# Kernel tuning notes

Hardware: AMD Instinct MI355X
Metric: run time of the kernel (lower is better)

## Reference

```python
import jax, jax.numpy as jnp
import numpy as np

B, T, E, H = 4, 4096, 1024, 64

def setup_inputs() -> dict:
    key = jax.random.key(0)
    kx, kk, kq, kv = jax.random.split(key, 4)
    x = jax.random.normal(kx, (B, T, E), dtype=jnp.float32)
    Wk = jax.random.normal(kk, (E, H), dtype=jnp.float32) * (E ** -0.5)
    Wq = jax.random.normal(kq, (E, H), dtype=jnp.float32) * (E ** -0.5)
    Wv = jax.random.normal(kv, (E, H), dtype=jnp.float32) * (E ** -0.5)
    return {"x": x, "Wk": Wk, "Wq": Wq, "Wv": Wv}

def reference(x, Wk, Wq, Wv):
    # x: [B, T, E]; single causal attention head, dropout rate 0 (no-op)
    t = x.shape[1]
    k = jnp.einsum('bte,eh->bth', x, Wk)  # [B,T,H]
    q = jnp.einsum('bte,eh->bth', x, Wq)  # [B,T,H]
    v = jnp.einsum('bte,eh->bth', x, Wv)  # [B,T,H]
    scores = jnp.einsum('bqh,bkh->bqk', q, k) * (k.shape[-1] ** -0.5)  # [B,T,T]
    causal = jnp.tril(jnp.ones((t, t), dtype=bool))
    scores = jnp.where(causal, scores, -jnp.inf)
    attn = jax.nn.softmax(scores, axis=-1)
    return jnp.einsum('bqk,bkh->bqh', attn, v)  # [B,T,H]
```

## Files before the change

kernel.cpp:

```cpp
#include <hip/hip_runtime.h>
#include <hip/hip_bf16.h>

typedef short short8 __attribute__((ext_vector_type(8)));
typedef short short4v __attribute__((ext_vector_type(4)));
typedef float float4v __attribute__((ext_vector_type(4)));
typedef float f32x4 __attribute__((ext_vector_type(4)));

#define NEG_HUGE (-1e30f)
#define QK_SCALE 0.1803368801111204f

__device__ __forceinline__ unsigned short f2bf(float f) {
  union { __hip_bfloat16 h; unsigned short u; } c;
  c.h = __float2bfloat16(f);
  return c.u;
}

#define MFMA16(a, b, c) __builtin_amdgcn_mfma_f32_16x16x32_bf16((a), (b), (c), 0, 0, 0)

__global__ __launch_bounds__(256) void wtrans_kernel(
    const float* __restrict__ Wk, const float* __restrict__ Wq,
    const float* __restrict__ Wv, unsigned short* __restrict__ Wt) {
  int mat = blockIdx.x >> 4, kb = blockIdx.x & 15;
  const float* W = (mat == 0) ? Wk : ((mat == 1) ? Wq : Wv);
  float qscale = (mat == 1) ? QK_SCALE : 1.0f;
  __shared__ float tile[64][65];
  int tid = threadIdx.x;
  int n = tid & 63, k0 = tid >> 6;
#pragma unroll
  for (int i = 0; i < 16; i++) {
    int k = i * 4 + k0;
    tile[k][n] = W[(kb * 64 + k) * 64 + n];
  }
  __syncthreads();
  int n2 = tid >> 2, c = tid & 3;
  unsigned short tmp[16];
#pragma unroll
  for (int j = 0; j < 16; j++) tmp[j] = f2bf(tile[c * 16 + j][n2] * qscale);
  unsigned short* dst = Wt + (mat * 64 + n2) * 1024 + kb * 64 + c * 16;
  *(short8*)dst = *(short8*)tmp;
  *(short8*)(dst + 8) = *(short8*)(tmp + 8);
}

__global__ __launch_bounds__(256, 4) void proj_kernel(
    const float* __restrict__ x, const unsigned short* __restrict__ Wt,
    unsigned short* __restrict__ Kb, unsigned short* __restrict__ Qb,
    unsigned short* __restrict__ Vt) {
  __shared__ unsigned short x_lds[32][40];
  __shared__ unsigned short w_lds[192][40];
  int tid = threadIdx.x;
  int w = tid >> 6, lane = tid & 63;
  int wm = w & 1, wn = w >> 1;
  int g = lane >> 4, r = lane & 15;
  int row0 = blockIdx.x * 32;

  int xr = tid >> 3, c4 = tid & 7;
  const float* xp = &x[(size_t)(row0 + xr) * 1024 + c4 * 4];

  f32x4 acc[6];
#pragma unroll
  for (int nf = 0; nf < 6; nf++) acc[nf] = (f32x4){0.f, 0.f, 0.f, 0.f};

  float4v xv = *(const float4v*)xp;
  short8 wv[3];
#pragma unroll
  for (int i = 0; i < 3; i++) {
    int idx = tid + i * 256;
    int wr = idx >> 2, c = idx & 3;
    wv[i] = *(const short8*)&Wt[wr * 1024 + c * 8];
  }

  for (int k0 = 0; k0 < 1024; k0 += 32) {
    {
      unsigned short t4[4];
      t4[0] = f2bf(xv[0]); t4[1] = f2bf(xv[1]); t4[2] = f2bf(xv[2]); t4[3] = f2bf(xv[3]);
      *(short4v*)&x_lds[xr][c4 * 4] = *(short4v*)t4;
    }
#pragma unroll
    for (int i = 0; i < 3; i++) {
      int idx = tid + i * 256;
      int wr = idx >> 2, c = idx & 3;
      *(short8*)&w_lds[wr][c * 8] = wv[i];
    }
    if (k0 + 32 < 1024) {
      xv = *(const float4v*)(xp + k0 + 32);
#pragma unroll
      for (int i = 0; i < 3; i++) {
        int idx = tid + i * 256;
        int wr = idx >> 2, c = idx & 3;
        wv[i] = *(const short8*)&Wt[wr * 1024 + k0 + 32 + c * 8];
      }
    }
    __syncthreads();
    short8 a = *(short8*)&x_lds[wm * 16 + r][g * 8];
#pragma unroll
    for (int nf = 0; nf < 6; nf++) {
      short8 bf = *(short8*)&w_lds[wn * 96 + nf * 16 + r][g * 8];
      acc[nf] = MFMA16(a, bf, acc[nf]);
    }
    __syncthreads();
  }
#pragma unroll
  for (int nf = 0; nf < 6; nf++) {
    int col = wn * 96 + nf * 16 + r;
    if (col < 128) {
      int mat = col >> 6, h = col & 63;
      unsigned short* dst = (mat == 0) ? Kb : Qb;
#pragma unroll
      for (int reg = 0; reg < 4; reg++) {
        int grow = row0 + wm * 16 + g * 4 + reg;
        dst[(size_t)grow * 64 + h] = f2bf(acc[nf][reg]);
      }
    } else {
      int h = col & 63;
      int grow0 = row0 + wm * 16 + g * 4;
      unsigned short t4[4];
#pragma unroll
      for (int reg = 0; reg < 4; reg++) t4[reg] = f2bf(acc[nf][reg]);
      int kv6 = grow0 & 63;
      int nfb = (kv6 >> 4) & 3, gb = (kv6 >> 2) & 3;
      int s0 = (nfb >> 1) * 32 + gb * 8 + (nfb & 1) * 4;
      size_t off = ((size_t)(grow0 >> 12) * 64 + h) * 4096 +
                   ((size_t)(grow0 & 4095) & ~(size_t)63) + s0;
      *(short4v*)&Vt[off] = *(short4v*)t4;
    }
  }
}

__global__ __launch_bounds__(256, 3) void attn_kernel(
    const unsigned short* __restrict__ Kb, const unsigned short* __restrict__ Qb,
    const unsigned short* __restrict__ VtB, float* __restrict__ out) {
  __shared__ float O_l[4][32][68];
  __shared__ float st_l[4][32][2];
  int tid = threadIdx.x;
  int w = tid >> 6, lane = tid & 63;
  int g = lane >> 4, r = lane & 15;
  int bi = blockIdx.x;
  int b = bi & 3, iq = bi >> 2;
  int qt = (iq < 64) ? (64 + iq) : (127 - iq);
  int qabs = qt * 32;
  const unsigned short* Kp = Kb + (size_t)b * 4096 * 64;
  const unsigned short* Qp = Qb + (size_t)b * 4096 * 64;
  const unsigned short* Vp = VtB + (size_t)b * 64 * 4096;

  short8 qa[2][2];
#pragma unroll
  for (int mf = 0; mf < 2; mf++)
#pragma unroll
    for (int ks = 0; ks < 2; ks++)
      qa[mf][ks] = *(const short8*)&Qp[(size_t)(qabs + mf * 16 + r) * 64 + ks * 32 + g * 8];

  float m_st[2] = {NEG_HUGE, NEG_HUGE};
  float l_ln[2] = {0.f, 0.f};
  f32x4 o[4][2];
#pragma unroll
  for (int nfh = 0; nfh < 4; nfh++)
#pragma unroll
    for (int mf = 0; mf < 2; mf++) o[nfh][mf] = (f32x4){0.f, 0.f, 0.f, 0.f};

  int ntiles = (qabs >> 6) + 1;
  for (int t = w; t < ntiles; t += 4) {
    int kvb = t << 6;
    f32x4 s[4][2];
#pragma unroll
    for (int nf = 0; nf < 4; nf++)
#pragma unroll
      for (int mf = 0; mf < 2; mf++) s[nf][mf] = (f32x4){0.f, 0.f, 0.f, 0.f};
#pragma unroll
    for (int ks = 0; ks < 2; ks++) {
      short8 kf[4];
#pragma unroll
      for (int nf = 0; nf < 4; nf++)
        kf[nf] = *(const short8*)&Kp[(size_t)(kvb + nf * 16 + r) * 64 + ks * 32 + g * 8];
#pragma unroll
      for (int nf = 0; nf < 4; nf++) {
        s[nf][0] = MFMA16(kf[nf], qa[0][ks], s[nf][0]);
        s[nf][1] = MFMA16(kf[nf], qa[1][ks], s[nf][1]);
      }
    }
    short8 vf[2][4];
#pragma unroll
    for (int ks = 0; ks < 2; ks++)
#pragma unroll
      for (int nfh = 0; nfh < 4; nfh++)
        vf[ks][nfh] = *(const short8*)&Vp[(size_t)(nfh * 16 + r) * 4096 + kvb + ks * 32 + g * 8];
    if (kvb + 63 > qabs) {
#pragma unroll
      for (int mf = 0; mf < 2; mf++) {
        int q = qabs + mf * 16 + r;
#pragma unroll
        for (int nf = 0; nf < 4; nf++)
#pragma unroll
          for (int reg = 0; reg < 4; reg++) {
            int kv = kvb + nf * 16 + g * 4 + reg;
            if (kv > q) s[nf][mf][reg] = NEG_HUGE;
          }
      }
    }
    float alpha[2];
#pragma unroll
    for (int mf = 0; mf < 2; mf++) {
      float m0 = fmaxf(fmaxf(fmaxf(s[0][mf][0], s[0][mf][1]), fmaxf(s[0][mf][2], s[0][mf][3])),
                       fmaxf(fmaxf(s[1][mf][0], s[1][mf][1]), fmaxf(s[1][mf][2], s[1][mf][3])));
      float m1 = fmaxf(fmaxf(fmaxf(s[2][mf][0], s[2][mf][1]), fmaxf(s[2][mf][2], s[2][mf][3])),
                       fmaxf(fmaxf(s[3][mf][0], s[3][mf][1]), fmaxf(s[3][mf][2], s[3][mf][3])));
      float m0a = fmaxf(m0, m1);
      m0a = fmaxf(m0a, __shfl_xor(m0a, 16));
      m0a = fmaxf(m0a, __shfl_xor(m0a, 32));
      float mn = fmaxf(m_st[mf], m0a);
      alpha[mf] = exp2f(m_st[mf] - mn);
      m_st[mf] = mn;
    }
#pragma unroll
    for (int mf = 0; mf < 2; mf++) {
      float rs = 0.f;
#pragma unroll
      for (int nf = 0; nf < 4; nf++)
#pragma unroll
        for (int reg = 0; reg < 4; reg++) {
          float p = exp2f(s[nf][mf][reg] - m_st[mf]);
          s[nf][mf][reg] = p;
          rs += p;
        }
      l_ln[mf] = l_ln[mf] * alpha[mf] + rs;
#pragma unroll
      for (int nfh = 0; nfh < 4; nfh++)
#pragma unroll
        for (int reg = 0; reg < 4; reg++) o[nfh][mf][reg] *= alpha[mf];
    }
#pragma unroll
    for (int ks = 0; ks < 2; ks++)
#pragma unroll
      for (int mf = 0; mf < 2; mf++) {
        union { unsigned u[4]; short8 v; } pb;
        asm("v_cvt_pk_bf16_f32 %0, %1, %2" : "=v"(pb.u[0]) : "v"(s[2 * ks][mf][0]), "v"(s[2 * ks][mf][1]));
        asm("v_cvt_pk_bf16_f32 %0, %1, %2" : "=v"(pb.u[1]) : "v"(s[2 * ks][mf][2]), "v"(s[2 * ks][mf][3]));
        asm("v_cvt_pk_bf16_f32 %0, %1, %2" : "=v"(pb.u[2]) : "v"(s[2 * ks + 1][mf][0]), "v"(s[2 * ks + 1][mf][1]));
        asm("v_cvt_pk_bf16_f32 %0, %1, %2" : "=v"(pb.u[3]) : "v"(s[2 * ks + 1][mf][2]), "v"(s[2 * ks + 1][mf][3]));
#pragma unroll
        for (int nfh = 0; nfh < 4; nfh++)
          o[nfh][mf] = MFMA16(vf[ks][nfh], pb.v, o[nfh][mf]);
      }
  }
#pragma unroll
  for (int mf = 0; mf < 2; mf++) {
    float s0 = l_ln[mf];
    s0 += __shfl_xor(s0, 16);
    s0 += __shfl_xor(s0, 32);
    l_ln[mf] = s0;
  }
  __syncthreads();
#pragma unroll
  for (int nfh = 0; nfh < 4; nfh++)
#pragma unroll
    for (int mf = 0; mf < 2; mf++)
      *(f32x4*)&O_l[w][mf * 16 + r][nfh * 16 + g * 4] = o[nfh][mf];
  if (g == 0) {
#pragma unroll
    for (int mf = 0; mf < 2; mf++) {
      st_l[w][mf * 16 + r][0] = m_st[mf];
      st_l[w][mf * 16 + r][1] = l_ln[mf];
    }
  }
  __syncthreads();
  {
    int row = tid >> 3, cg = tid & 7;
    float mw[4], lw[4];
#pragma unroll
    for (int ww = 0; ww < 4; ww++) {
      mw[ww] = st_l[ww][row][0];
      lw[ww] = st_l[ww][row][1];
    }
    float mstar = fmaxf(fmaxf(mw[0], mw[1]), fmaxf(mw[2], mw[3]));
    float sc[4], lstar = 0.f;
#pragma unroll
    for (int ww = 0; ww < 4; ww++) { sc[ww] = exp2f(mw[ww] - mstar); lstar += sc[ww] * lw[ww]; }
    float inv = 1.0f / lstar;
    float a0[8];
#pragma unroll
    for (int cc = 0; cc < 8; cc++) a0[cc] = 0.f;
#pragma unroll
    for (int ww = 0; ww < 4; ww++) {
      f32x4 v0 = *(f32x4*)&O_l[ww][row][cg * 8];
      f32x4 v1 = *(f32x4*)&O_l[ww][row][cg * 8 + 4];
#pragma unroll
      for (int e = 0; e < 4; e++) { a0[e] += sc[ww] * v0[e]; a0[4 + e] += sc[ww] * v1[e]; }
    }
    float4v o0, o1;
#pragma unroll
    for (int e = 0; e < 4; e++) { o0[e] = a0[e] * inv; o1[e] = a0[4 + e] * inv; }
    float* op = &out[((size_t)b * 4096 + qabs + row) * 64 + cg * 8];
    *(float4v*)op = o0;
    *(float4v*)(op + 4) = o1;
  }
}

extern "C" void kernel_launch(void* const* d_in, const int* in_sizes, int n_in,
                              void* d_out, int out_size, void* d_ws, size_t ws_size,
                              hipStream_t stream) {
  (void)in_sizes; (void)n_in; (void)out_size; (void)ws_size;
  const float* x  = (const float*)d_in[0];
  const float* Wk = (const float*)d_in[1];
  const float* Wq = (const float*)d_in[2];
  const float* Wv = (const float*)d_in[3];
  float* out = (float*)d_out;
  char* ws = (char*)d_ws;

  unsigned short* Wt = (unsigned short*)ws;
  unsigned short* Kb = (unsigned short*)(ws + (512u << 10));
  unsigned short* Qb = (unsigned short*)(ws + (512u << 10) + (2u << 20));
  unsigned short* Vt = (unsigned short*)(ws + (512u << 10) + (4u << 20));

  wtrans_kernel<<<48, 256, 0, stream>>>(Wk, Wq, Wv, Wt);
  proj_kernel<<<512, 256, 0, stream>>>(x, Wt, Kb, Qb, Vt);
  attn_kernel<<<512, 256, 0, stream>>>(Kb, Qb, Vt, out);
}
```

Baseline: 62.96 us.

## Double-buffer LDS in projection kernel and widen K step to 64

Moves the QKV projection GEMM to double-buffered LDS tiles with a 64-wide K step. This halves the iteration count and needs one barrier per iteration instead of two. The next tile's global loads are issued before the MFMAs on the current tile and written to the alternate buffer afterwards, overlapping memory latency with compute. It raises LDS use and register pressure, so launch bounds drop to 2 blocks per CU.

```diff
diff --git a/kernel.cpp b/kernel.cpp
--- a/kernel.cpp
+++ b/kernel.cpp
@@ -41,61 +41,79 @@
   *(short8*)(dst + 8) = *(short8*)(tmp + 8);
 }
 
-__global__ __launch_bounds__(256, 4) void proj_kernel(
+__global__ __launch_bounds__(256, 2) void proj_kernel(
     const float* __restrict__ x, const unsigned short* __restrict__ Wt,
     unsigned short* __restrict__ Kb, unsigned short* __restrict__ Qb,
     unsigned short* __restrict__ Vt) {
-  __shared__ unsigned short x_lds[32][40];
-  __shared__ unsigned short w_lds[192][40];
+  __shared__ unsigned short x_lds[2][32][68];
+  __shared__ unsigned short w_lds[2][192][68];
   int tid = threadIdx.x;
   int w = tid >> 6, lane = tid & 63;
   int wm = w & 1, wn = w >> 1;
   int g = lane >> 4, r = lane & 15;
   int row0 = blockIdx.x * 32;
 
-  int xr = tid >> 3, c4 = tid & 7;
-  const float* xp = &x[(size_t)(row0 + xr) * 1024 + c4 * 4];
+  int xr = tid >> 3, xc8 = tid & 7;
+  const float* xp = &x[(size_t)(row0 + xr) * 1024 + xc8 * 8];
+  int wr[6], wc8[6];
+#pragma unroll
+  for (int i = 0; i < 6; i++) {
+    int idx = tid + i * 256;
+    wr[i] = idx >> 3;
+    wc8[i] = idx & 7;
+  }
 
   f32x4 acc[6];
 #pragma unroll
   for (int nf = 0; nf < 6; nf++) acc[nf] = (f32x4){0.f, 0.f, 0.f, 0.f};
 
-  float4v xv = *(const float4v*)xp;
-  short8 wv[3];
-#pragma unroll
-  for (int i = 0; i < 3; i++) {
-    int idx = tid + i * 256;
-    int wr = idx >> 2, c = idx & 3;
-    wv[i] = *(const short8*)&Wt[wr * 1024 + c * 8];
-  }
-
-  for (int k0 = 0; k0 < 1024; k0 += 32) {
-    {
-      unsigned short t4[4];
-      t4[0] = f2bf(xv[0]); t4[1] = f2bf(xv[1]); t4[2] = f2bf(xv[2]); t4[3] = f2bf(xv[3]);
-      *(short4v*)&x_lds[xr][c4 * 4] = *(short4v*)t4;
-    }
-#pragma unroll
-    for (int i = 0; i < 3; i++) {
-      int idx = tid + i * 256;
-      int wr = idx >> 2, c = idx & 3;
-      *(short8*)&w_lds[wr][c * 8] = wv[i];
-    }
-    if (k0 + 32 < 1024) {
-      xv = *(const float4v*)(xp + k0 + 32);
-#pragma unroll
-      for (int i = 0; i < 3; i++) {
-        int idx = tid + i * 256;
-        int wr = idx >> 2, c = idx & 3;
-        wv[i] = *(const short8*)&Wt[wr * 1024 + k0 + 32 + c * 8];
-      }
-    }
-    __syncthreads();
-    short8 a = *(short8*)&x_lds[wm * 16 + r][g * 8];
+  float4v xv0, xv1;
+  short8 wv[6];
+
+  xv0 = *(const float4v*)(xp + 0);
+  xv1 = *(const float4v*)(xp + 4);
+#pragma unroll
+  for (int i = 0; i < 6; i++)
+    wv[i] = *(const short8*)&Wt[wr[i] * 1024 + wc8[i] * 8];
+
+  {
+    unsigned short t8[8];
+    t8[0] = f2bf(xv0[0]); t8[1] = f2bf(xv0[1]); t8[2] = f2bf(xv0[2]); t8[3] = f2bf(xv0[3]);
+    t8[4] = f2bf(xv1[0]); t8[5] = f2bf(xv1[1]); t8[6] = f2bf(xv1[2]); t8[7] = f2bf(xv1[3]);
+    *(short8*)&x_lds[0][xr][xc8 * 8] = *(short8*)t8;
+#pragma unroll
+    for (int i = 0; i < 6; i++)
+      *(short8*)&w_lds[0][wr[i]][wc8[i] * 8] = wv[i];
+  }
+  __syncthreads();
+
+  for (int t = 0; t < 16; t++) {
+    int cur = t & 1;
+    if (t < 15) {
+      int k0 = (t + 1) * 64;
+      xv0 = *(const float4v*)(xp + k0);
+      xv1 = *(const float4v*)(xp + k0 + 4);
+#pragma unroll
+      for (int i = 0; i < 6; i++)
+        wv[i] = *(const short8*)&Wt[wr[i] * 1024 + k0 + wc8[i] * 8];
+    }
+    short8 a0 = *(short8*)&x_lds[cur][wm * 16 + r][g * 8];
+    short8 a1 = *(short8*)&x_lds[cur][wm * 16 + r][32 + g * 8];
 #pragma unroll
     for (int nf = 0; nf < 6; nf++) {
-      short8 bf = *(short8*)&w_lds[wn * 96 + nf * 16 + r][g * 8];
-      acc[nf] = MFMA16(a, bf, acc[nf]);
+      short8 b0 = *(short8*)&w_lds[cur][wn * 96 + nf * 16 + r][g * 8];
+      short8 b1 = *(short8*)&w_lds[cur][wn * 96 + nf * 16 + r][32 + g * 8];
+      acc[nf] = MFMA16(a0, b0, acc[nf]);
+      acc[nf] = MFMA16(a1, b1, acc[nf]);
+    }
+    if (t < 15) {
+      unsigned short t8[8];
+      t8[0] = f2bf(xv0[0]); t8[1] = f2bf(xv0[1]); t8[2] = f2bf(xv0[2]); t8[3] = f2bf(xv0[3]);
+      t8[4] = f2bf(xv1[0]); t8[5] = f2bf(xv1[1]); t8[6] = f2bf(xv1[2]); t8[7] = f2bf(xv1[3]);
+      *(short8*)&x_lds[cur ^ 1][xr][xc8 * 8] = *(short8*)t8;
+#pragma unroll
+      for (int i = 0; i < 6; i++)
+        *(short8*)&w_lds[cur ^ 1][wr[i]][wc8[i] * 8] = wv[i];
     }
     __syncthreads();
   }
```

Result: no change. 61.88 us (-1.7%).

## Load projection MFMA fragments directly from global memory, bypassing LDS

Applied to the files above, without the earlier changes.

The projection kernel stops staging x and W tiles through shared memory with two barriers per k-step. Each lane now loads its own MFMA A and B fragments straight from global memory, with register double-buffering and an unrolled loop. This removes LDS traffic and syncs, at the cost of redundant global and L2 reads: x rows are re-read by the wn waves and W rows by every block, and the per-lane strided accesses may coalesce less well.

```diff
diff --git a/kernel.cpp b/kernel.cpp
--- a/kernel.cpp
+++ b/kernel.cpp
@@ -45,59 +45,52 @@
     const float* __restrict__ x, const unsigned short* __restrict__ Wt,
     unsigned short* __restrict__ Kb, unsigned short* __restrict__ Qb,
     unsigned short* __restrict__ Vt) {
-  __shared__ unsigned short x_lds[32][40];
-  __shared__ unsigned short w_lds[192][40];
   int tid = threadIdx.x;
   int w = tid >> 6, lane = tid & 63;
   int wm = w & 1, wn = w >> 1;
   int g = lane >> 4, r = lane & 15;
   int row0 = blockIdx.x * 32;
 
-  int xr = tid >> 3, c4 = tid & 7;
-  const float* xp = &x[(size_t)(row0 + xr) * 1024 + c4 * 4];
+  const float* xp = &x[(size_t)(row0 + wm * 16 + r) * 1024 + g * 8];
+  const unsigned short* wp[6];
+#pragma unroll
+  for (int nf = 0; nf < 6; nf++)
+    wp[nf] = &Wt[(size_t)(wn * 96 + nf * 16 + r) * 1024 + g * 8];
 
   f32x4 acc[6];
 #pragma unroll
   for (int nf = 0; nf < 6; nf++) acc[nf] = (f32x4){0.f, 0.f, 0.f, 0.f};
 
-  float4v xv = *(const float4v*)xp;
-  short8 wv[3];
-#pragma unroll
-  for (int i = 0; i < 3; i++) {
-    int idx = tid + i * 256;
-    int wr = idx >> 2, c = idx & 3;
-    wv[i] = *(const short8*)&Wt[wr * 1024 + c * 8];
-  }
-
-  for (int k0 = 0; k0 < 1024; k0 += 32) {
-    {
-      unsigned short t4[4];
-      t4[0] = f2bf(xv[0]); t4[1] = f2bf(xv[1]); t4[2] = f2bf(xv[2]); t4[3] = f2bf(xv[3]);
-      *(short4v*)&x_lds[xr][c4 * 4] = *(short4v*)t4;
-    }
-#pragma unroll
-    for (int i = 0; i < 3; i++) {
-      int idx = tid + i * 256;
-      int wr = idx >> 2, c = idx & 3;
-      *(short8*)&w_lds[wr][c * 8] = wv[i];
-    }
-    if (k0 + 32 < 1024) {
-      xv = *(const float4v*)(xp + k0 + 32);
-#pragma unroll
-      for (int i = 0; i < 3; i++) {
-        int idx = tid + i * 256;
-        int wr = idx >> 2, c = idx & 3;
-        wv[i] = *(const short8*)&Wt[wr * 1024 + k0 + 32 + c * 8];
-      }
-    }
-    __syncthreads();
-    short8 a = *(short8*)&x_lds[wm * 16 + r][g * 8];
-#pragma unroll
-    for (int nf = 0; nf < 6; nf++) {
-      short8 bf = *(short8*)&w_lds[wn * 96 + nf * 16 + r][g * 8];
-      acc[nf] = MFMA16(a, bf, acc[nf]);
-    }
-    __syncthreads();
+  float4v a_lo = *(const float4v*)(xp);
+  float4v a_hi = *(const float4v*)(xp + 4);
+  short8 bc[6];
+#pragma unroll
+  for (int nf = 0; nf < 6; nf++) bc[nf] = *(const short8*)(wp[nf]);
+
+#pragma unroll 4
+  for (int k = 0; k < 992; k += 32) {
+    float4v n_lo = *(const float4v*)(xp + k + 32);
+    float4v n_hi = *(const float4v*)(xp + k + 36);
+    short8 bn[6];
+#pragma unroll
+    for (int nf = 0; nf < 6; nf++) bn[nf] = *(const short8*)(wp[nf] + k + 32);
+    unsigned short t8[8];
+    t8[0] = f2bf(a_lo[0]); t8[1] = f2bf(a_lo[1]); t8[2] = f2bf(a_lo[2]); t8[3] = f2bf(a_lo[3]);
+    t8[4] = f2bf(a_hi[0]); t8[5] = f2bf(a_hi[1]); t8[6] = f2bf(a_hi[2]); t8[7] = f2bf(a_hi[3]);
+    short8 af = *(short8*)t8;
+#pragma unroll
+    for (int nf = 0; nf < 6; nf++) acc[nf] = MFMA16(af, bc[nf], acc[nf]);
+    a_lo = n_lo; a_hi = n_hi;
+#pragma unroll
+    for (int nf = 0; nf < 6; nf++) bc[nf] = bn[nf];
+  }
+  {
+    unsigned short t8[8];
+    t8[0] = f2bf(a_lo[0]); t8[1] = f2bf(a_lo[1]); t8[2] = f2bf(a_lo[2]); t8[3] = f2bf(a_lo[3]);
+    t8[4] = f2bf(a_hi[0]); t8[5] = f2bf(a_hi[1]); t8[6] = f2bf(a_hi[2]); t8[7] = f2bf(a_hi[3]);
+    short8 af = *(short8*)t8;
+#pragma unroll
+    for (int nf = 0; nf < 6; nf++) acc[nf] = MFMA16(af, bc[nf], acc[nf]);
   }
 #pragma unroll
   for (int nf = 0; nf < 6; nf++) {
```

Result: slower. 101.7 us (+61.5%).

## Retile projection kernel to 64-row blocks with double-buffered swizzled LDS

Applied to the files above, without the earlier changes.

The projection kernel now processes 64 rows per 512-thread block with a K-step of 64, halving the number of K iterations. It double-buffers the LDS tiles, which removes the second barrier per iteration, and uses an XOR swizzle instead of padding to avoid bank conflicts. The goal is to cut synchronization overhead and the re-reading of W per row. The trade-off is more LDS per block and fewer blocks (256) to spread across the GPU.

```diff
diff --git a/kernel.cpp b/kernel.cpp
--- a/kernel.cpp
+++ b/kernel.cpp
@@ -41,63 +41,69 @@
   *(short8*)(dst + 8) = *(short8*)(tmp + 8);
 }
 
-__global__ __launch_bounds__(256, 4) void proj_kernel(
+__global__ __launch_bounds__(512, 2) void proj_kernel(
     const float* __restrict__ x, const unsigned short* __restrict__ Wt,
     unsigned short* __restrict__ Kb, unsigned short* __restrict__ Qb,
     unsigned short* __restrict__ Vt) {
-  __shared__ unsigned short x_lds[32][40];
-  __shared__ unsigned short w_lds[192][40];
+  __shared__ unsigned short x_l[2][64 * 64];
+  __shared__ unsigned short w_l[2][192 * 64];
   int tid = threadIdx.x;
   int w = tid >> 6, lane = tid & 63;
-  int wm = w & 1, wn = w >> 1;
+  int wm = w >> 1, wn = w & 1;
   int g = lane >> 4, r = lane & 15;
-  int row0 = blockIdx.x * 32;
-
-  int xr = tid >> 3, c4 = tid & 7;
-  const float* xp = &x[(size_t)(row0 + xr) * 1024 + c4 * 4];
+  int row0 = blockIdx.x * 64;
+
+  int xr = tid >> 3, xc16 = tid & 7;
+  const float* xp = &x[(size_t)(row0 + xr) * 1024 + xc16 * 8];
+  int xelem = xr * 64 + ((xc16 * 8) ^ ((xr & 7) << 3));
+  const unsigned short* wp[3];
+  int welem[3];
+#pragma unroll
+  for (int i = 0; i < 3; i++) {
+    int c = tid + i * 512;
+    int wr = c >> 3, wc16 = c & 7;
+    wp[i] = &Wt[(size_t)wr * 1024 + wc16 * 8];
+    welem[i] = wr * 64 + ((wc16 * 8) ^ ((wr & 7) << 3));
+  }
+  int swz = (r & 7) << 3;
 
   f32x4 acc[6];
 #pragma unroll
   for (int nf = 0; nf < 6; nf++) acc[nf] = (f32x4){0.f, 0.f, 0.f, 0.f};
 
-  float4v xv = *(const float4v*)xp;
+  float4v xa = *(const float4v*)(xp);
+  float4v xb = *(const float4v*)(xp + 4);
   short8 wv[3];
 #pragma unroll
-  for (int i = 0; i < 3; i++) {
-    int idx = tid + i * 256;
-    int wr = idx >> 2, c = idx & 3;
-    wv[i] = *(const short8*)&Wt[wr * 1024 + c * 8];
-  }
-
-  for (int k0 = 0; k0 < 1024; k0 += 32) {
+  for (int i = 0; i < 3; i++) wv[i] = *(const short8*)(wp[i]);
+
+  for (int t = 0; t < 16; t++) {
+    int buf = t & 1;
     {
-      unsigned short t4[4];
-      t4[0] = f2bf(xv[0]); t4[1] = f2bf(xv[1]); t4[2] = f2bf(xv[2]); t4[3] = f2bf(xv[3]);
-      *(short4v*)&x_lds[xr][c4 * 4] = *(short4v*)t4;
-    }
-#pragma unroll
-    for (int i = 0; i < 3; i++) {
-      int idx = tid + i * 256;
-      int wr = idx >> 2, c = idx & 3;
-      *(short8*)&w_lds[wr][c * 8] = wv[i];
-    }
-    if (k0 + 32 < 1024) {
-      xv = *(const float4v*)(xp + k0 + 32);
-#pragma unroll
-      for (int i = 0; i < 3; i++) {
-        int idx = tid + i * 256;
-        int wr = idx >> 2, c = idx & 3;
-        wv[i] = *(const short8*)&Wt[wr * 1024 + k0 + 32 + c * 8];
-      }
+      unsigned short t8[8];
+      t8[0] = f2bf(xa[0]); t8[1] = f2bf(xa[1]); t8[2] = f2bf(xa[2]); t8[3] = f2bf(xa[3]);
+      t8[4] = f2bf(xb[0]); t8[5] = f2bf(xb[1]); t8[6] = f2bf(xb[2]); t8[7] = f2bf(xb[3]);
+      *(short8*)&x_l[buf][xelem] = *(short8*)t8;
+#pragma unroll
+      for (int i = 0; i < 3; i++) *(short8*)&w_l[buf][welem[i]] = wv[i];
+    }
+    if (t < 15) {
+      int k0 = (t + 1) * 64;
+      xa = *(const float4v*)(xp + k0);
+      xb = *(const float4v*)(xp + k0 + 4);
+#pragma unroll
+      for (int i = 0; i < 3; i++) wv[i] = *(const short8*)(wp[i] + k0);
     }
     __syncthreads();
-    short8 a = *(short8*)&x_lds[wm * 16 + r][g * 8];
-#pragma unroll
-    for (int nf = 0; nf < 6; nf++) {
-      short8 bf = *(short8*)&w_lds[wn * 96 + nf * 16 + r][g * 8];
-      acc[nf] = MFMA16(a, bf, acc[nf]);
-    }
-    __syncthreads();
+#pragma unroll
+    for (int ks = 0; ks < 2; ks++) {
+      short8 af = *(short8*)&x_l[buf][(wm * 16 + r) * 64 + ((ks * 32 + g * 8) ^ swz)];
+#pragma unroll
+      for (int nf = 0; nf < 6; nf++) {
+        short8 bf = *(short8*)&w_l[buf][(wn * 96 + nf * 16 + r) * 64 + ((ks * 32 + g * 8) ^ swz)];
+        acc[nf] = MFMA16(af, bf, acc[nf]);
+      }
+    }
   }
 #pragma unroll
   for (int nf = 0; nf < 6; nf++) {
@@ -311,6 +317,6 @@
   unsigned short* Vt = (unsigned short*)(ws + (512u << 10) + (4u << 20));
 
   wtrans_kernel<<<48, 256, 0, stream>>>(Wk, Wq, Wv, Wt);
-  proj_kernel<<<512, 256, 0, stream>>>(x, Wt, Kb, Qb, Vt);
+  proj_kernel<<<256, 512, 0, stream>>>(x, Wt, Kb, Qb, Vt);
   attn_kernel<<<512, 256, 0, stream>>>(Kb, Qb, Vt, out);
 }
```

New measurement: 56.63 us. -10.1%, faster.
